# Optimization experiments

Measured on AMD Instinct MI355X. Metric: run time of the kernel, lower is better.

Reference implementation:

```python
import jax, jax.numpy as jnp
import numpy as np

B = 16384   # number of cells
SD = 1024   # spatial_dim
TD = 1024   # temporal_dim
FD = 1024   # fusion_dim
H = 8       # num_attention_heads


def setup_inputs() -> dict:
    key = jax.random.key(0)
    ks = jax.random.split(key, 40)
    it = iter(range(40))

    def w(o, i):
        return jax.random.normal(ks[next(it)], (o, i), dtype=jnp.float32) * 0.02

    def b(o):
        return jnp.zeros((o,), dtype=jnp.float32)

    d = {
        "spatial_features": jax.random.normal(ks[next(it)], (B, SD), dtype=jnp.float32),
        "temporal_features": jax.random.normal(ks[next(it)], (B, TD), dtype=jnp.float32),
        "sp_w": w(FD, SD), "sp_b": b(FD),
        "tp_w": w(FD, TD), "tp_b": b(FD),
    }
    for pre in ("st", "ts", "sa"):  # spatial->temporal, temporal->spatial, self
        for nm in ("q", "k", "v", "o"):
            d[f"{pre}_{nm}w"] = w(FD, FD)
            d[f"{pre}_{nm}b"] = b(FD)
    d["f1_w"] = w(FD, 2 * FD); d["f1_b"] = b(FD)
    d["f2_w"] = w(FD, FD);     d["f2_b"] = b(FD)
    d["ln_g"] = jnp.ones((FD,), jnp.float32)
    d["ln_b"] = jnp.zeros((FD,), jnp.float32)
    return d


def _mha(xq, xk, xv, qw, qb, kw, kb, vw, vb, ow, ob):
    # xq: [B, Lq, D]; xk/xv: [B, Lk, D]
    Bx, Lq, D = xq.shape
    Lk = xk.shape[1]
    hd = D // H
    Q = (xq @ qw.T + qb).reshape(Bx, Lq, H, hd)
    K = (xk @ kw.T + kb).reshape(Bx, Lk, H, hd)
    V = (xv @ vw.T + vb).reshape(Bx, Lk, H, hd)
    scores = jnp.einsum("bqhd,bkhd->bhqk", Q, K) / jnp.sqrt(jnp.float32(hd))
    attn = jax.nn.softmax(scores, axis=-1)
    out = jnp.einsum("bhqk,bkhd->bqhd", attn, V).reshape(Bx, Lq, D)
    return out @ ow.T + ob


def reference(spatial_features, temporal_features,
              sp_w, sp_b, tp_w, tp_b,
              st_qw, st_qb, st_kw, st_kb, st_vw, st_vb, st_ow, st_ob,
              ts_qw, ts_qb, ts_kw, ts_kb, ts_vw, ts_vb, ts_ow, ts_ob,
              sa_qw, sa_qb, sa_kw, sa_kb, sa_vw, sa_vb, sa_ow, sa_ob,
              f1_w, f1_b, f2_w, f2_b, ln_g, ln_b):
    # projections to fusion dim, add seq_len=1 axis
    sp = (spatial_features @ sp_w.T + sp_b)[:, None, :]   # [B,1,F]
    tp = (temporal_features @ tp_w.T + tp_b)[:, None, :]  # [B,1,F]

    # cross attention
    s_att = _mha(sp, tp, tp, st_qw, st_qb, st_kw, st_kb, st_vw, st_vb, st_ow, st_ob)[:, 0, :]
    t_att = _mha(tp, sp, sp, ts_qw, ts_qb, ts_kw, ts_kb, ts_vw, ts_vb, ts_ow, ts_ob)[:, 0, :]

    # concat fusion MLP
    cat = jnp.concatenate([s_att, t_att], axis=-1)        # [B,2F]
    fused = jax.nn.relu(cat @ f1_w.T + f1_b) @ f2_w.T + f2_b

    # self attention over seq_len=1
    fe = fused[:, None, :]
    fused = _mha(fe, fe, fe, sa_qw, sa_qb, sa_kw, sa_kb, sa_vw, sa_vb, sa_ow, sa_ob)[:, 0, :]

    # layer norm (eps matches torch default 1e-5)
    mu = jnp.mean(fused, axis=-1, keepdims=True)
    var = jnp.mean(jnp.square(fused - mu), axis=-1, keepdims=True)
    return (fused - mu) * jax.lax.rsqrt(var + 1e-5) * ln_g + ln_b
```

## Files before the change

kernel.cpp:

```cpp
#include <hip/hip_runtime.h>
#include <hip/hip_fp16.h>


typedef _Float16 half8 __attribute__((ext_vector_type(8)));
typedef float floatx4 __attribute__((ext_vector_type(4)));

#define GLOBAL_AS __attribute__((address_space(1)))
#define LDS_AS __attribute__((address_space(3)))

#define NB 16384
#define FDIM 1024

#define SBAR() asm volatile("s_barrier" ::: "memory")
#define WAIT_LGKM0() asm volatile("s_waitcnt lgkmcnt(0)" ::: "memory")
#define WAIT_VM(n) asm volatile("s_waitcnt vmcnt(" #n ")" ::: "memory")
#define DSREAD(dst, addr) asm volatile("ds_read_b128 %0, %1" : "=v"(dst) : "v"(addr))

template <int RELU>
__global__ __launch_bounds__(512, 2) void gemm256(
    const _Float16* __restrict__ A, const _Float16* __restrict__ W,
    const float* __restrict__ bias, _Float16* __restrict__ C,
    int M, int N, int K, int ldc) {
  __shared__ __align__(16) _Float16 smem[2 * 2 * 256 * 64];

  const int t = threadIdx.x;
  const int lane = t & 63;
  const int w = t >> 6;
  const int wr = w >> 2;
  const int wc = w & 3;

  const int nwg = gridDim.x;
  const int bid = blockIdx.x;
  const int swz = (bid & 7) * (nwg >> 3) + (bid >> 3);
  const int nTN = N >> 8;
  const int m0 = (swz / nTN) << 8;
  const int n0 = (swz % nTN) << 8;
  const int NT = K >> 6;

  const int srow = w * 16 + (lane >> 3);
  const int scs = (lane & 7) ^ ((lane >> 3) & 7);
  const char* gA = (const char*)(A + (long)(m0 + srow) * K + scs * 8);
  const char* gB = (const char*)(W + (long)(n0 + srow) * K + scs * 8);
  const long dJ = (long)K * 16;
  const long dH = (long)K * 256;
  const int ldst = w * 2048 + lane * 16;

  unsigned sb = (unsigned)(unsigned long long)(LDS_AS void*)smem;
  const int frow = lane & 15;
  const unsigned offk = (unsigned)((((lane >> 4) * 16) ^ ((frow & 7) << 4)));
  const unsigned aoff = (unsigned)((wr * 128 + frow) * 128);
  const unsigned boff = (unsigned)(32768 + (wc * 64 + frow) * 128);

  floatx4 acc[8][4] = {};

#define STAGE(ab, hf, buf, gp, kb)                                               \
  do {                                                                           \
    const char* _s = (gp) + (hf) * dH + (kb);                                    \
    char* _d = (char*)smem + (buf) * 65536 + (ab) * 32768 + (hf) * 16384 + ldst; \
    __builtin_amdgcn_global_load_lds((const GLOBAL_AS void*)_s,                  \
                                     (LDS_AS void*)_d, 16, 0, 0);                \
    __builtin_amdgcn_global_load_lds((const GLOBAL_AS void*)(_s + dJ),           \
                                     (LDS_AS void*)(_d + 1024), 16, 0, 0);       \
  } while (0)

#define QUAD(a0, a1, i0, i1)                                                              \
  do {                                                                                    \
    __builtin_amdgcn_s_setprio(1);                                                       \
    _Pragma("unroll") for (int c = 0; c < 4; ++c) {                                      \
      acc[i0][c] = __builtin_amdgcn_mfma_f32_16x16x32_f16(a0[0], b[c][0], acc[i0][c], 0, 0, 0); \
      acc[i0][c] = __builtin_amdgcn_mfma_f32_16x16x32_f16(a0[1], b[c][1], acc[i0][c], 0, 0, 0); \
      acc[i1][c] = __builtin_amdgcn_mfma_f32_16x16x32_f16(a1[0], b[c][0], acc[i1][c], 0, 0, 0); \
      acc[i1][c] = __builtin_amdgcn_mfma_f32_16x16x32_f16(a1[1], b[c][1], acc[i1][c], 0, 0, 0); \
    }                                                                                     \
    __builtin_amdgcn_s_setprio(0);                                                       \
  } while (0)

  {
    const long k1 = 128L;
    STAGE(0, 0, 0, gA, 0); STAGE(0, 1, 0, gA, 0);
    STAGE(1, 0, 0, gB, 0); STAGE(1, 1, 0, gB, 0);
    STAGE(1, 0, 1, gB, k1); STAGE(1, 1, 1, gB, k1);
  }
  WAIT_VM(4);
  SBAR();

  for (int kt = 0; kt < NT; ++kt) {
    const int cur = kt & 1, nxt = cur ^ 1;
    const unsigned baseA = sb + (unsigned)(cur * 65536) + aoff;
    const unsigned baseB = sb + (unsigned)(cur * 65536) + boff;
    const long kb1 = (long)(kt + 1 < NT ? kt + 1 : NT - 1) * 128;
    const long kb2 = (long)(kt + 2 < NT ? kt + 2 : NT - 1) * 128;

    half8 b[4][2], alo[4][2], ahi[4][2];

#pragma unroll
    for (int c = 0; c < 4; ++c) {
      DSREAD(b[c][0], baseB + c * 2048 + offk);
      DSREAD(b[c][1], baseB + c * 2048 + (offk ^ 64u));
    }
#pragma unroll
    for (int r = 0; r < 2; ++r) {
      DSREAD(alo[r][0], baseA + r * 2048 + offk);
      DSREAD(alo[r][1], baseA + r * 2048 + (offk ^ 64u));
    }
    STAGE(0, 0, nxt, gA, kb1);
    SBAR();
    WAIT_LGKM0();
    __builtin_amdgcn_sched_barrier(0);
    QUAD(alo[0], alo[1], 0, 1);
    SBAR();

#pragma unroll
    for (int r = 2; r < 4; ++r) {
      DSREAD(alo[r][0], baseA + r * 2048 + offk);
      DSREAD(alo[r][1], baseA + r * 2048 + (offk ^ 64u));
    }
    STAGE(0, 1, nxt, gA, kb1);
    SBAR();
    WAIT_LGKM0();
    __builtin_amdgcn_sched_barrier(0);
    QUAD(alo[2], alo[3], 2, 3);
    SBAR();

#pragma unroll
    for (int r = 0; r < 2; ++r) {
      DSREAD(ahi[r][0], baseA + (r + 4) * 2048 + offk);
      DSREAD(ahi[r][1], baseA + (r + 4) * 2048 + (offk ^ 64u));
    }
    STAGE(1, 0, cur, gB, kb2);
    SBAR();
    WAIT_LGKM0();
    __builtin_amdgcn_sched_barrier(0);
    QUAD(ahi[0], ahi[1], 4, 5);
    SBAR();

#pragma unroll
    for (int r = 2; r < 4; ++r) {
      DSREAD(ahi[r][0], baseA + (r + 4) * 2048 + offk);
      DSREAD(ahi[r][1], baseA + (r + 4) * 2048 + (offk ^ 64u));
    }
    STAGE(1, 1, cur, gB, kb2);
    WAIT_VM(4);
    SBAR();
    WAIT_LGKM0();
    __builtin_amdgcn_sched_barrier(0);
    QUAD(ahi[2], ahi[3], 6, 7);
    SBAR();
  }
  WAIT_VM(0);

  const int rbase = (lane >> 4) * 4;
#pragma unroll
  for (int c = 0; c < 4; ++c) {
    const int col = n0 + wc * 64 + c * 16 + frow;
    const float bv = bias[col];
#pragma unroll
    for (int r = 0; r < 8; ++r) {
#pragma unroll
      for (int j = 0; j < 4; ++j) {
        int row = m0 + wr * 128 + r * 16 + rbase + j;
        float v = acc[r][c][j] + bv;
        if (RELU) v = fmaxf(v, 0.f);
        C[(long)row * ldc + col] = (_Float16)v;
      }
    }
  }
#undef STAGE
#undef QUAD
}

struct CVE { const float* in; _Float16* out; long ld_in; long ld_out; long n4; };
struct CVB { CVE e[7]; };
__global__ __launch_bounds__(256) void cvt_batch(CVB a) {
  const CVE e = a.e[blockIdx.y];
  long i = (long)blockIdx.x * blockDim.x + threadIdx.x;
  long stride = (long)gridDim.x * blockDim.x;
  for (; i < e.n4; i += stride) {
    long row = i >> 8;
    long c4 = i & 255;
    float4 v = *reinterpret_cast<const float4*>(e.in + row * e.ld_in + c4 * 4);
    union { _Float16 h[4]; short4 s; } u;
    u.h[0] = (_Float16)v.x; u.h[1] = (_Float16)v.y;
    u.h[2] = (_Float16)v.z; u.h[3] = (_Float16)v.w;
    *reinterpret_cast<short4*>(e.out + row * e.ld_out + c4 * 4) = u.s;
  }
}

struct TP8 { const float* in[8]; _Float16* out[8]; };
__global__ __launch_bounds__(256) void transpose_cvt(TP8 args) {
  __shared__ float tile[32][33];
  const float* in = args.in[blockIdx.z];
  _Float16* out = args.out[blockIdx.z];
  const int bx = blockIdx.x * 32;
  const int by = blockIdx.y * 32;
  const int tx = threadIdx.x & 31;
  const int ty = threadIdx.x >> 5;
#pragma unroll
  for (int r = 0; r < 32; r += 8)
    tile[ty + r][tx] = in[(long)(by + ty + r) * 1024 + bx + tx];
  __syncthreads();
#pragma unroll
  for (int r = 0; r < 32; r += 8)
    out[(long)(bx + ty + r) * 1024 + by + tx] = (_Float16)tile[tx][ty + r];
}

struct MVE { const float* W; const float* x; const float* add; float* y; long ld; int kj; };
struct MVB { MVE e[3]; };
__global__ __launch_bounds__(256) void matvecb(MVB a) {
  const MVE e = a.e[blockIdx.y];
  const int row = blockIdx.x * 4 + (threadIdx.x >> 6);
  const int lane = threadIdx.x & 63;
  const float* wr = e.W + (long)row * e.ld;
  float s = 0.f;
  for (int j = 0; j < e.kj; ++j) {
    float4 w4 = *reinterpret_cast<const float4*>(wr + (lane + 64 * j) * 4);
    float4 x4 = *reinterpret_cast<const float4*>(e.x + (lane + 64 * j) * 4);
    s += w4.x * x4.x + w4.y * x4.y + w4.z * x4.z + w4.w * x4.w;
  }
#pragma unroll
  for (int off = 32; off > 0; off >>= 1) s += __shfl_down(s, off);
  if (lane == 0) e.y[row] = s + (e.add ? e.add[row] : 0.f);
}

struct GemmArgs { const _Float16* A; const _Float16* W; const float* bias; _Float16* C; int ldc; };
struct GB5 { GemmArgs g[5]; };

__global__ __launch_bounds__(256, 2) void gemm_f16(GB5 args, int M, int N, int K) {
  __shared__ __align__(16) _Float16 As[128 * 32];
  __shared__ __align__(16) _Float16 Ws[128 * 32];

  const GemmArgs ga = args.g[blockIdx.y];
  const int t = threadIdx.x;
  const int lane = t & 63;
  const int wave = t >> 6;
  const int wr = wave >> 1;
  const int wc = wave & 1;

  const int nwg = gridDim.x;
  const int bid = blockIdx.x;
  const int swz = (bid & 7) * (nwg >> 3) + (bid >> 3);
  const int nTilesN = N >> 7;
  const int m0 = (swz / nTilesN) << 7;
  const int n0 = (swz % nTilesN) << 7;

  floatx4 acc[4][4] = {};
  const int srow = t >> 2;
  const int scol = (t & 3) * 8;
  const _Float16* Ag = ga.A + (long)(m0 + srow) * K + scol;
  const _Float16* Wg = ga.W + (long)(n0 + srow) * K + scol;
  const int frow = lane & 15;
  const int fk = (lane >> 4) * 8;

  for (int k0 = 0; k0 < K; k0 += 32) {
#pragma unroll
    for (int i = 0; i < 2; ++i) {
      __builtin_amdgcn_global_load_lds(
          (const GLOBAL_AS void*)(Ag + (long)i * 64 * K + k0),
          (LDS_AS void*)(&As[i * 2048 + t * 8]), 16, 0, 0);
      __builtin_amdgcn_global_load_lds(
          (const GLOBAL_AS void*)(Wg + (long)i * 64 * K + k0),
          (LDS_AS void*)(&Ws[i * 2048 + t * 8]), 16, 0, 0);
    }
    __syncthreads();
    half8 a[4], b[4];
#pragma unroll
    for (int r = 0; r < 4; ++r)
      a[r] = *(const half8*)&As[(wr * 64 + r * 16 + frow) * 32 + fk];
#pragma unroll
    for (int c = 0; c < 4; ++c)
      b[c] = *(const half8*)&Ws[(wc * 64 + c * 16 + frow) * 32 + fk];
#pragma unroll
    for (int r = 0; r < 4; ++r)
#pragma unroll
      for (int c = 0; c < 4; ++c)
        acc[r][c] = __builtin_amdgcn_mfma_f32_16x16x32_f16(a[r], b[c], acc[r][c], 0, 0, 0);
    __syncthreads();
  }

  const int rbase = lane >> 4;
#pragma unroll
  for (int c = 0; c < 4; ++c) {
    const int col = n0 + wc * 64 + c * 16 + frow;
    const float bv = ga.bias ? ga.bias[col] : 0.f;
#pragma unroll
    for (int r = 0; r < 4; ++r)
#pragma unroll
      for (int j = 0; j < 4; ++j) {
        int row = m0 + wr * 64 + r * 16 + rbase * 4 + j;
        ga.C[(long)row * ga.ldc + col] = (_Float16)(acc[r][c][j] + bv);
      }
  }
}

__global__ __launch_bounds__(256) void ln_f16(const _Float16* __restrict__ x,
                                              const float* __restrict__ g,
                                              const float* __restrict__ b,
                                              float* __restrict__ out) {
  const int row = blockIdx.x;
  const int t = threadIdx.x;
  const _Float16* xr = x + (size_t)row * FDIM;
  short4 raw = reinterpret_cast<const short4*>(xr)[t];
  union { short4 s; _Float16 h[4]; } u;
  u.s = raw;
  float v0 = (float)u.h[0], v1 = (float)u.h[1], v2 = (float)u.h[2], v3 = (float)u.h[3];
  float s = v0 + v1 + v2 + v3;
  float q = v0 * v0 + v1 * v1 + v2 * v2 + v3 * v3;
#pragma unroll
  for (int off = 32; off > 0; off >>= 1) {
    s += __shfl_down(s, off);
    q += __shfl_down(q, off);
  }
  __shared__ float ss[4], qs[4];
  int wave = t >> 6, lane = t & 63;
  if (lane == 0) { ss[wave] = s; qs[wave] = q; }
  __syncthreads();
  float S = ss[0] + ss[1] + ss[2] + ss[3];
  float Q = qs[0] + qs[1] + qs[2] + qs[3];
  float mu = S * (1.f / FDIM);
  float var = Q * (1.f / FDIM) - mu * mu;
  float rs = rsqrtf(var + 1e-5f);
  int c = t * 4;
  float4 o;
  o.x = (v0 - mu) * rs * g[c + 0] + b[c + 0];
  o.y = (v1 - mu) * rs * g[c + 1] + b[c + 1];
  o.z = (v2 - mu) * rs * g[c + 2] + b[c + 2];
  o.w = (v3 - mu) * rs * g[c + 3] + b[c + 3];
  reinterpret_cast<float4*>(out + (size_t)row * FDIM)[t] = o;
}

extern "C" void kernel_launch(void* const* d_in, const int* in_sizes, int n_in,
                              void* d_out, int out_size, void* d_ws, size_t ws_size,
                              hipStream_t stream) {
  const float* spatial  = (const float*)d_in[0];
  const float* temporal = (const float*)d_in[1];
  const float* sp_w = (const float*)d_in[2];
  const float* sp_b = (const float*)d_in[3];
  const float* tp_w = (const float*)d_in[4];
  const float* tp_b = (const float*)d_in[5];
  const float* st_vw = (const float*)d_in[10];
  const float* st_vb = (const float*)d_in[11];
  const float* st_ow = (const float*)d_in[12];
  const float* st_ob = (const float*)d_in[13];
  const float* ts_vw = (const float*)d_in[18];
  const float* ts_vb = (const float*)d_in[19];
  const float* ts_ow = (const float*)d_in[20];
  const float* ts_ob = (const float*)d_in[21];
  const float* sa_vw = (const float*)d_in[26];
  const float* sa_vb = (const float*)d_in[27];
  const float* sa_ow = (const float*)d_in[28];
  const float* sa_ob = (const float*)d_in[29];
  const float* f1_w = (const float*)d_in[30];
  const float* f1_b = (const float*)d_in[31];
  const float* f2_w = (const float*)d_in[32];
  const float* f2_b = (const float*)d_in[33];
  const float* ln_g = (const float*)d_in[34];
  const float* ln_b = (const float*)d_in[35];

  char* base = (char*)d_ws;
  size_t off = 0;
  auto alloc = [&](size_t bytes) { void* p = base + off; off += (bytes + 255) & ~255ull; return p; };
  const size_t W16 = 1024 * 1024 * sizeof(_Float16);

  _Float16* Xcat = (_Float16*)alloc((size_t)NB * 2048 * 2);
  _Float16* h    = (_Float16*)alloc((size_t)NB * 1024 * 2);
  _Float16* opre = (_Float16*)alloc((size_t)NB * 1024 * 2);
  _Float16* st_owT = (_Float16*)alloc(W16);
  _Float16* ts_owT = (_Float16*)alloc(W16);
  _Float16* sa_vwT = (_Float16*)alloc(W16);
  _Float16* tp_wT  = (_Float16*)alloc(W16);
  _Float16* sp_wT  = (_Float16*)alloc(W16);
  _Float16* f2_wT  = (_Float16*)alloc(W16);
  _Float16* f1a16  = (_Float16*)alloc(W16);
  _Float16* f1b16  = (_Float16*)alloc(W16);
  _Float16* sa_ow16= (_Float16*)alloc(W16);
  _Float16* st_vw16= (_Float16*)alloc(W16);
  _Float16* ts_vw16= (_Float16*)alloc(W16);
  _Float16* P1 = (_Float16*)alloc(W16);
  _Float16* Q2 = (_Float16*)alloc(W16);
  _Float16* P3 = (_Float16*)alloc(W16);
  _Float16* Q4 = (_Float16*)alloc(W16);
  _Float16* P5 = (_Float16*)alloc(W16);
  _Float16* W2 = (_Float16*)alloc(W16);
  _Float16* Wh = (_Float16*)alloc((size_t)1024 * 2048 * 2);
  float* u1 = (float*)alloc(3 * 1024 * 4);
  float* u2 = (float*)alloc(3 * 1024 * 4);
  float* bh = (float*)alloc(1024 * 4);

  {
    CVB cb = {};
    cb.e[0] = { temporal, Xcat,        1024, 2048, (long)NB * 256 };
    cb.e[1] = { spatial,  Xcat + 1024, 1024, 2048, (long)NB * 256 };
    cb.e[2] = { f1_w,        f1a16,   2048, 1024, 1024 * 256 };
    cb.e[3] = { f1_w + 1024, f1b16,   2048, 1024, 1024 * 256 };
    cb.e[4] = { sa_ow,       sa_ow16, 1024, 1024, 1024 * 256 };
    cb.e[5] = { st_vw,       st_vw16, 1024, 1024, 1024 * 256 };
    cb.e[6] = { ts_vw,       ts_vw16, 1024, 1024, 1024 * 256 };
    cvt_batch<<<dim3(1024, 7), 256, 0, stream>>>(cb);
  }

  TP8 tp = {};
  tp.in[0] = st_ow; tp.out[0] = st_owT;
  tp.in[1] = ts_ow; tp.out[1] = ts_owT;
  tp.in[2] = sa_vw; tp.out[2] = sa_vwT;
  tp.in[3] = tp_w;  tp.out[3] = tp_wT;
  tp.in[4] = sp_w;  tp.out[4] = sp_wT;
  tp.in[5] = f2_w;  tp.out[5] = f2_wT;
  transpose_cvt<<<dim3(32, 32, 6), 256, 0, stream>>>(tp);

  {
    MVB a = {};
    a.e[0] = { st_vw, tp_b, st_vb, u1,        1024, 4 };
    a.e[1] = { ts_vw, sp_b, ts_vb, u1 + 1024, 1024, 4 };
    a.e[2] = { sa_vw, f2_b, sa_vb, u1 + 2048, 1024, 4 };
    matvecb<<<dim3(256, 3), 256, 0, stream>>>(a);
  }
  {
    MVB a = {};
    a.e[0] = { st_ow, u1,        st_ob, u2,        1024, 4 };
    a.e[1] = { ts_ow, u1 + 1024, ts_ob, u2 + 1024, 1024, 4 };
    a.e[2] = { sa_ow, u1 + 2048, sa_ob, u2 + 2048, 1024, 4 };
    matvecb<<<dim3(256, 3), 256, 0, stream>>>(a);
  }
  {
    MVB a = {};
    a.e[0] = { f1_w, u2, f1_b, bh, 2048, 8 };
    matvecb<<<dim3(256, 1), 256, 0, stream>>>(a);
  }

  {
    GB5 g = {};
    g.g[0] = { f1a16,  st_owT, nullptr, P1, 1024 };
    g.g[1] = { tp_wT,  st_vw16, nullptr, Q2, 1024 };
    g.g[2] = { f1b16,  ts_owT, nullptr, P3, 1024 };
    g.g[3] = { sp_wT,  ts_vw16, nullptr, Q4, 1024 };
    g.g[4] = { sa_ow16, sa_vwT, nullptr, P5, 1024 };
    gemm_f16<<<dim3(64, 5), 256, 0, stream>>>(g, 1024, 1024, 1024);
  }
  {
    GB5 g = {};
    g.g[0] = { P1, Q2, nullptr, Wh,        2048 };
    g.g[1] = { P3, Q4, nullptr, Wh + 1024, 2048 };
    g.g[2] = { P5, f2_wT, nullptr, W2,     1024 };
    gemm_f16<<<dim3(64, 3), 256, 0, stream>>>(g, 1024, 1024, 1024);
  }

  gemm256<1><<<dim3(256), 512, 0, stream>>>(Xcat, Wh, bh, h, NB, 1024, 2048, 1024);
  gemm256<0><<<dim3(256), 512, 0, stream>>>(h, W2, u2 + 2048, opre, NB, 1024, 1024, 1024);

  ln_f16<<<NB, 256, 0, stream>>>(opre, ln_g, ln_b, (float*)d_out);
}
```

Before: 234.1 us.

## Prefetch next A fragments from LDS while MFMAs run in the GEMM

```diff
diff --git a/kernel.cpp b/kernel.cpp
--- a/kernel.cpp
+++ b/kernel.cpp
@@ -14,6 +14,7 @@
 #define SBAR() asm volatile("s_barrier" ::: "memory")
 #define WAIT_LGKM0() asm volatile("s_waitcnt lgkmcnt(0)" ::: "memory")
 #define WAIT_VM(n) asm volatile("s_waitcnt vmcnt(" #n ")" ::: "memory")
+#define SB0() __builtin_amdgcn_sched_barrier(0)
 #define DSREAD(dst, addr) asm volatile("ds_read_b128 %0, %1" : "=v"(dst) : "v"(addr))
 
 template <int RELU>
@@ -52,6 +53,7 @@
   const unsigned boff = (unsigned)(32768 + (wc * 64 + frow) * 128);
 
   floatx4 acc[8][4] = {};
+  half8 b[4][2], aP[2][2], aQ[2][2];
 
 #define STAGE(ab, hf, buf, gp, kb)                                               \
   do {                                                                           \
@@ -63,16 +65,32 @@
                                      (LDS_AS void*)(_d + 1024), 16, 0, 0);       \
   } while (0)
 
-#define QUAD(a0, a1, i0, i1)                                                              \
-  do {                                                                                    \
-    __builtin_amdgcn_s_setprio(1);                                                       \
-    _Pragma("unroll") for (int c = 0; c < 4; ++c) {                                      \
-      acc[i0][c] = __builtin_amdgcn_mfma_f32_16x16x32_f16(a0[0], b[c][0], acc[i0][c], 0, 0, 0); \
-      acc[i0][c] = __builtin_amdgcn_mfma_f32_16x16x32_f16(a0[1], b[c][1], acc[i0][c], 0, 0, 0); \
-      acc[i1][c] = __builtin_amdgcn_mfma_f32_16x16x32_f16(a1[0], b[c][0], acc[i1][c], 0, 0, 0); \
-      acc[i1][c] = __builtin_amdgcn_mfma_f32_16x16x32_f16(a1[1], b[c][1], acc[i1][c], 0, 0, 0); \
-    }                                                                                     \
-    __builtin_amdgcn_s_setprio(0);                                                       \
+#define RD_B()                                                                    \
+  do {                                                                            \
+    _Pragma("unroll") for (int c = 0; c < 4; ++c) {                               \
+      DSREAD(b[c][0], baseB + c * 2048 + offk);                                   \
+      DSREAD(b[c][1], baseB + c * 2048 + (offk ^ 64u));                           \
+    }                                                                             \
+  } while (0)
+
+#define RD_A(S, r, ba)                                                            \
+  do {                                                                            \
+    DSREAD(S[0][0], (ba) + (r) * 2048 + offk);                                    \
+    DSREAD(S[0][1], (ba) + (r) * 2048 + (offk ^ 64u));                            \
+    DSREAD(S[1][0], (ba) + (r + 1) * 2048 + offk);                                \
+    DSREAD(S[1][1], (ba) + (r + 1) * 2048 + (offk ^ 64u));                        \
+  } while (0)
+
+#define QUAD(S, i0, i1)                                                                     \
+  do {                                                                                      \
+    __builtin_amdgcn_s_setprio(1);                                                          \
+    _Pragma("unroll") for (int c = 0; c < 4; ++c) {                                         \
+      acc[i0][c] = __builtin_amdgcn_mfma_f32_16x16x32_f16(S[0][0], b[c][0], acc[i0][c], 0, 0, 0); \
+      acc[i0][c] = __builtin_amdgcn_mfma_f32_16x16x32_f16(S[0][1], b[c][1], acc[i0][c], 0, 0, 0); \
+      acc[i1][c] = __builtin_amdgcn_mfma_f32_16x16x32_f16(S[1][0], b[c][0], acc[i1][c], 0, 0, 0); \
+      acc[i1][c] = __builtin_amdgcn_mfma_f32_16x16x32_f16(S[1][1], b[c][1], acc[i1][c], 0, 0, 0); \
+    }                                                                                       \
+    __builtin_amdgcn_s_setprio(0);                                                          \
   } while (0)
 
   {
@@ -83,71 +101,48 @@
   }
   WAIT_VM(4);
   SBAR();
+  RD_A(aP, 0, sb + aoff);
 
   for (int kt = 0; kt < NT; ++kt) {
     const int cur = kt & 1, nxt = cur ^ 1;
     const unsigned baseA = sb + (unsigned)(cur * 65536) + aoff;
+    const unsigned baseAn = sb + (unsigned)(nxt * 65536) + aoff;
     const unsigned baseB = sb + (unsigned)(cur * 65536) + boff;
     const long kb1 = (long)(kt + 1 < NT ? kt + 1 : NT - 1) * 128;
     const long kb2 = (long)(kt + 2 < NT ? kt + 2 : NT - 1) * 128;
 
-    half8 b[4][2], alo[4][2], ahi[4][2];
-
-#pragma unroll
-    for (int c = 0; c < 4; ++c) {
-      DSREAD(b[c][0], baseB + c * 2048 + offk);
-      DSREAD(b[c][1], baseB + c * 2048 + (offk ^ 64u));
-    }
-#pragma unroll
-    for (int r = 0; r < 2; ++r) {
-      DSREAD(alo[r][0], baseA + r * 2048 + offk);
-      DSREAD(alo[r][1], baseA + r * 2048 + (offk ^ 64u));
-    }
+    RD_B();
     STAGE(0, 0, nxt, gA, kb1);
+    SBAR(); WAIT_LGKM0();
+    RD_A(aQ, 2, baseA);
+    SB0();
+    QUAD(aP, 0, 1);
     SBAR();
-    WAIT_LGKM0();
-    __builtin_amdgcn_sched_barrier(0);
-    QUAD(alo[0], alo[1], 0, 1);
+
+    STAGE(0, 1, nxt, gA, kb1);
+    SBAR(); WAIT_LGKM0();
+    RD_A(aP, 4, baseA);
+    SB0();
+    QUAD(aQ, 2, 3);
     SBAR();
 
-#pragma unroll
-    for (int r = 2; r < 4; ++r) {
-      DSREAD(alo[r][0], baseA + r * 2048 + offk);
-      DSREAD(alo[r][1], baseA + r * 2048 + (offk ^ 64u));
-    }
-    STAGE(0, 1, nxt, gA, kb1);
+    STAGE(1, 0, cur, gB, kb2);
+    SBAR(); WAIT_LGKM0();
+    RD_A(aQ, 6, baseA);
+    SB0();
+    QUAD(aP, 4, 5);
     SBAR();
-    WAIT_LGKM0();
-    __builtin_amdgcn_sched_barrier(0);
-    QUAD(alo[2], alo[3], 2, 3);
-    SBAR();
-
-#pragma unroll
-    for (int r = 0; r < 2; ++r) {
-      DSREAD(ahi[r][0], baseA + (r + 4) * 2048 + offk);
-      DSREAD(ahi[r][1], baseA + (r + 4) * 2048 + (offk ^ 64u));
-    }
-    STAGE(1, 0, cur, gB, kb2);
-    SBAR();
-    WAIT_LGKM0();
-    __builtin_amdgcn_sched_barrier(0);
-    QUAD(ahi[0], ahi[1], 4, 5);
-    SBAR();
-
-#pragma unroll
-    for (int r = 2; r < 4; ++r) {
-      DSREAD(ahi[r][0], baseA + (r + 4) * 2048 + offk);
-      DSREAD(ahi[r][1], baseA + (r + 4) * 2048 + (offk ^ 64u));
-    }
+
     STAGE(1, 1, cur, gB, kb2);
     WAIT_VM(4);
+    SBAR(); WAIT_LGKM0();
+    RD_A(aP, 0, baseAn);
+    SB0();
+    QUAD(aQ, 6, 7);
     SBAR();
-    WAIT_LGKM0();
-    __builtin_amdgcn_sched_barrier(0);
-    QUAD(ahi[2], ahi[3], 6, 7);
-    SBAR();
   }
   WAIT_VM(0);
+  WAIT_LGKM0();
 
   const int rbase = (lane >> 4) * 4;
 #pragma unroll
@@ -166,6 +161,8 @@
     }
   }
 #undef STAGE
+#undef RD_B
+#undef RD_A
 #undef QUAD
 }
 
```

New measurement: 233.9 us. Within noise of the previous version (-0.1%).
